# Kernel optimization log

Measured on AMD Instinct MI355X. Metric: run time of the kernel, lower is better.

Reference implementation:

```python
import jax, jax.numpy as jnp
import numpy as np

N_U, N_P, E, E_LAB = 100000, 50000, 2000000, 500000
D_U, D_P, H = 64, 128, 64


def _seg_mean(feat, idx, n):
    # scatter-mean: sum per destination / clamp(count, 1)
    s = jax.ops.segment_sum(feat, idx, num_segments=n)
    c = jax.ops.segment_sum(jnp.ones((idx.shape[0],), feat.dtype), idx, num_segments=n)
    return s / jnp.maximum(c, 1.0)[:, None]


def setup_inputs() -> dict:
    key = jax.random.key(0)
    ks = jax.random.split(key, 16)
    inp = {
        'x_user': jax.random.normal(ks[0], (N_U, D_U), jnp.float32),
        'x_product': jax.random.normal(ks[1], (N_P, D_P), jnp.float32),
        'W1_buys_l': jax.random.normal(ks[2], (D_U, H), jnp.float32) * 0.05,
        'b1_buys': jnp.zeros((H,), jnp.float32),
        'W1_buys_r': jax.random.normal(ks[3], (D_P, H), jnp.float32) * 0.05,
        'W1_rev_l': jax.random.normal(ks[4], (D_P, H), jnp.float32) * 0.05,
        'b1_rev': jnp.zeros((H,), jnp.float32),
        'W1_rev_r': jax.random.normal(ks[5], (D_U, H), jnp.float32) * 0.05,
        'W2_buys_l': jax.random.normal(ks[6], (H, H), jnp.float32) * 0.05,
        'b2_buys': jnp.zeros((H,), jnp.float32),
        'W2_buys_r': jax.random.normal(ks[7], (H, H), jnp.float32) * 0.05,
        'W2_rev_l': jax.random.normal(ks[8], (H, H), jnp.float32) * 0.05,
        'b2_rev': jnp.zeros((H,), jnp.float32),
        'W2_rev_r': jax.random.normal(ks[9], (H, H), jnp.float32) * 0.05,
        'edge_src': jax.random.randint(ks[10], (E,), 0, N_U, jnp.int32),
        'edge_dst': jax.random.randint(ks[11], (E,), 0, N_P, jnp.int32),
        'lab_u': jax.random.randint(ks[12], (E_LAB,), 0, N_U, jnp.int32),
        'lab_p': jax.random.randint(ks[13], (E_LAB,), 0, N_P, jnp.int32),
    }
    return inp


def reference(x_user, x_product, W1_buys_l, b1_buys, W1_buys_r, W1_rev_l, b1_rev, W1_rev_r,
              W2_buys_l, b2_buys, W2_buys_r, W2_rev_l, b2_rev, W2_rev_r,
              edge_src, edge_dst, lab_u, lab_p):
    # SAGEConv (mean aggr): out_dst = mean_agg(x_src) @ W_l + b + x_dst @ W_r
    def sage(x_src, x_dst, src, dst, n_dst, Wl, b, Wr):
        agg = _seg_mean(x_src[src], dst, n_dst)
        return agg @ Wl + b + x_dst @ Wr

    n_u, n_p = x_user.shape[0], x_product.shape[0]
    # layer 1 (per edge type, hetero) + relu
    h_p = jax.nn.relu(sage(x_user, x_product, edge_src, edge_dst, n_p, W1_buys_l, b1_buys, W1_buys_r))
    h_u = jax.nn.relu(sage(x_product, x_user, edge_dst, edge_src, n_u, W1_rev_l, b1_rev, W1_rev_r))
    # layer 2
    h_p2 = sage(h_u, h_p, edge_src, edge_dst, n_p, W2_buys_l, b2_buys, W2_buys_r)
    h_u2 = sage(h_p, h_u, edge_dst, edge_src, n_u, W2_rev_l, b2_rev, W2_rev_r)
    # classifier: per-label-edge dot product
    return jnp.sum(h_u2[lab_u] * h_p2[lab_p], axis=-1)
```

## Files before the change

kernel.cpp:

```cpp
#include <hip/hip_runtime.h>


using u16 = unsigned short;
using u32 = unsigned int;

__device__ __forceinline__ u16 bf16r(float f) {
    u32 b = __float_as_uint(f);
    b += 0x7fffu + ((b >> 16) & 1u);
    return (u16)(b >> 16);
}
__device__ __forceinline__ float bflo(u32 u) { return __uint_as_float(u << 16); }
__device__ __forceinline__ float bfhi(u32 u) { return __uint_as_float(u & 0xffff0000u); }

#define BSH 8
#define MAXB 512
#define CHUNK 4096
#define RPT 16

__global__ __launch_bounds__(256) void k_histA(const int* __restrict__ esrc,
                                               const int* __restrict__ edst,
                                               int* __restrict__ bcntP,
                                               int* __restrict__ bcntU,
                                               int NBP, int NBU, int E) {
    __shared__ int hP[MAXB];
    __shared__ int hU[MAXB];
    int tid = threadIdx.x;
    for (int i = tid; i < MAXB; i += 256) { hP[i] = 0; hU[i] = 0; }
    __syncthreads();
    int E4 = E >> 2;
    const int4* s4 = (const int4*)esrc;
    const int4* d4 = (const int4*)edst;
    int stride = gridDim.x * 256;
    for (int i = blockIdx.x * 256 + tid; i < E4; i += stride) {
        int4 s = s4[i], d = d4[i];
        atomicAdd(&hU[s.x >> BSH], 1); atomicAdd(&hU[s.y >> BSH], 1);
        atomicAdd(&hU[s.z >> BSH], 1); atomicAdd(&hU[s.w >> BSH], 1);
        atomicAdd(&hP[d.x >> BSH], 1); atomicAdd(&hP[d.y >> BSH], 1);
        atomicAdd(&hP[d.z >> BSH], 1); atomicAdd(&hP[d.w >> BSH], 1);
    }
    if (blockIdx.x == 0 && tid < (E & 3)) {
        int e = E4 * 4 + tid;
        atomicAdd(&hU[esrc[e] >> BSH], 1);
        atomicAdd(&hP[edst[e] >> BSH], 1);
    }
    __syncthreads();
    for (int i = tid; i < NBP; i += 256) if (hP[i]) atomicAdd(&bcntP[i], hP[i]);
    for (int i = tid; i < NBU; i += 256) if (hU[i]) atomicAdd(&bcntU[i], hU[i]);
}

__global__ __launch_bounds__(256) void k_scanBuckets(const int* __restrict__ cntP,
                                                     int* __restrict__ basesP,
                                                     int* __restrict__ curP, int NBP,
                                                     const int* __restrict__ cntU,
                                                     int* __restrict__ basesU,
                                                     int* __restrict__ curU, int NBU) {
    const int* cnt; int* bases; int* cur; int NB;
    if (blockIdx.x == 0) { cnt = cntP; bases = basesP; cur = curP; NB = NBP; }
    else                 { cnt = cntU; bases = basesU; cur = curU; NB = NBU; }
    __shared__ int sA[MAXB];
    __shared__ int sB[MAXB];
    int tid = threadIdx.x;
    int v0 = (tid < NB) ? cnt[tid] : 0;
    int v1 = (tid + 256 < NB) ? cnt[tid + 256] : 0;
    sA[tid] = v0; sA[tid + 256] = v1;
    __syncthreads();
    int* src = sA; int* dst = sB;
    for (int off = 1; off < MAXB; off <<= 1) {
        dst[tid] = src[tid] + ((tid >= off) ? src[tid - off] : 0);
        int i2 = tid + 256;
        dst[i2] = src[i2] + ((i2 >= off) ? src[i2 - off] : 0);
        __syncthreads();
        int* t = src; src = dst; dst = t;
    }
    if (tid < NB)       { bases[tid] = src[tid] - v0;             cur[tid] = src[tid] - v0; }
    if (tid + 256 < NB) { bases[tid + 256] = src[tid + 256] - v1; cur[tid + 256] = src[tid + 256] - v1; }
    if (tid == 0) bases[NB] = src[MAXB - 1];
}

__global__ __launch_bounds__(256) void k_partition(const int* __restrict__ keys,
                                                   const int* __restrict__ payload,
                                                   int* __restrict__ cursor,
                                                   uint2* __restrict__ pairs,
                                                   int NB, int E) {
    __shared__ int hist[MAXB];
    __shared__ int sA[MAXB];
    __shared__ int sB[MAXB];
    __shared__ int bx[MAXB];
    __shared__ int gbase[MAXB];
    __shared__ uint2 prs[CHUNK];
    int tid = threadIdx.x;
    int i0 = blockIdx.x * CHUNK;
    int count = min(CHUNK, E - i0);
    for (int i = tid; i < MAXB; i += 256) hist[i] = 0;
    __syncthreads();
    int keyr[RPT], payr[RPT], rankr[RPT];
#pragma unroll
    for (int r = 0; r < RPT; ++r) {
        int idx = r * 256 + tid;
        if (idx < count) {
            int k = keys[i0 + idx];
            keyr[r] = k;
            payr[r] = payload[i0 + idx];
            rankr[r] = atomicAdd(&hist[k >> BSH], 1);
        } else keyr[r] = -1;
    }
    __syncthreads();
    sA[tid] = hist[tid]; sA[tid + 256] = hist[tid + 256];
    __syncthreads();
    int* src = sA; int* dst = sB;
    for (int off = 1; off < MAXB; off <<= 1) {
        dst[tid] = src[tid] + ((tid >= off) ? src[tid - off] : 0);
        int i2 = tid + 256;
        dst[i2] = src[i2] + ((i2 >= off) ? src[i2 - off] : 0);
        __syncthreads();
        int* t = src; src = dst; dst = t;
    }
    bx[tid] = src[tid] - hist[tid];
    bx[tid + 256] = src[tid + 256] - hist[tid + 256];
    __syncthreads();
    for (int b = tid; b < NB; b += 256) {
        int c = hist[b];
        gbase[b] = c ? atomicAdd(&cursor[b], c) : 0;
    }
#pragma unroll
    for (int r = 0; r < RPT; ++r) {
        if (keyr[r] >= 0)
            prs[bx[keyr[r] >> BSH] + rankr[r]] = make_uint2((u32)keyr[r], (u32)payr[r]);
    }
    __syncthreads();
    for (int j = tid; j < count; j += 256) {
        uint2 pr = prs[j];
        int b = pr.x >> BSH;
        pairs[gbase[b] + (j - bx[b])] = pr;
    }
}

__global__ __launch_bounds__(256) void k_bucketFill(
    const uint2* __restrict__ pairsP, const int* __restrict__ basesP, int NBP,
    int* __restrict__ nbr_p, int* __restrict__ deg_p, int* __restrict__ ptr_p, int NP,
    const uint2* __restrict__ pairsU, const int* __restrict__ basesU, int NBU,
    int* __restrict__ nbr_u, int* __restrict__ deg_u, int* __restrict__ ptr_u, int NU) {
    const uint2* pairs; const int* bases; int* nbr; int* deg; int* ptr; int N; int bucket;
    if ((int)blockIdx.x < NBP) {
        pairs = pairsP; bases = basesP; nbr = nbr_p; deg = deg_p; ptr = ptr_p; N = NP;
        bucket = blockIdx.x;
    } else {
        pairs = pairsU; bases = basesU; nbr = nbr_u; deg = deg_u; ptr = ptr_u; N = NU;
        bucket = blockIdx.x - NBP;
    }
    int tid = threadIdx.x;
    int base = bases[bucket];
    int cnt = bases[bucket + 1] - base;
    __shared__ int h[256];
    __shared__ int s[256];
    __shared__ int cur[256];
    h[tid] = 0;
    __syncthreads();
    for (int j = tid; j < cnt; j += 256) atomicAdd(&h[pairs[base + j].x & 255], 1);
    __syncthreads();
    int d = h[tid];
    s[tid] = d;
    __syncthreads();
    for (int off = 1; off < 256; off <<= 1) {
        int v = (tid >= off) ? s[tid - off] : 0;
        __syncthreads();
        s[tid] += v;
        __syncthreads();
    }
    int excl = s[tid] - d;
    int node = bucket * 256 + tid;
    if (node < N) { deg[node] = d; ptr[node] = base + excl; }
    cur[tid] = excl;
    __syncthreads();
    for (int j = tid; j < cnt; j += 256) {
        uint2 pr = pairs[base + j];
        int pos = atomicAdd(&cur[pr.x & 255], 1);
        nbr[base + pos] = pr.y;
    }
}

__global__ __launch_bounds__(256) void k_cast8(const float* __restrict__ x,
                                               u16* __restrict__ y, int n8) {
    int i = blockIdx.x * 256 + threadIdx.x;
    if (i >= n8) return;
    const float4* x4 = (const float4*)x;
    float4 a = x4[i * 2], b = x4[i * 2 + 1];
    uint4 o;
    o.x = (u32)bf16r(a.x) | ((u32)bf16r(a.y) << 16);
    o.y = (u32)bf16r(a.z) | ((u32)bf16r(a.w) << 16);
    o.z = (u32)bf16r(b.x) | ((u32)bf16r(b.y) << 16);
    o.w = (u32)bf16r(b.z) | ((u32)bf16r(b.w) << 16);
    ((uint4*)y)[i] = o;
}

#define ACC8(A0,A1,A2,A3,A4,A5,A6,A7,V) \
    A0 += bflo((V).x); A1 += bfhi((V).x); A2 += bflo((V).y); A3 += bfhi((V).y); \
    A4 += bflo((V).z); A5 += bfhi((V).z); A6 += bflo((V).w); A7 += bfhi((V).w);

__global__ __launch_bounds__(256) void k_gather2(
    const u16* __restrict__ yA, const int* __restrict__ nbrA, const int* __restrict__ stpA,
    const int* __restrict__ degA, float* __restrict__ aggA, int NA,
    const u16* __restrict__ yB, const int* __restrict__ nbrB, const int* __restrict__ stpB,
    const int* __restrict__ degB, float* __restrict__ aggB, int NB) {
    int w = (blockIdx.x * 256 + threadIdx.x) >> 6;
    int lane = threadIdx.x & 63;
    if (w >= NA + NB) return;
    const u16* y; const int* nbr; const int* stp; const int* deg; float* agg; int n;
    if (w < NA) { y = yA; nbr = nbrA; stp = stpA; deg = degA; agg = aggA; n = w; }
    else        { y = yB; nbr = nbrB; stp = stpB; deg = degB; agg = aggB; n = w - NA; }
    const int q = lane >> 3, t = lane & 7;
    const int d = deg[n];
    int j = stp[n];
    const int end = j + d;
    float a0=0,a1=0,a2=0,a3=0,a4=0,a5=0,a6=0,a7=0;
    float b0=0,b1=0,b2=0,b3=0,b4=0,b5=0,b6=0,b7=0;
    float c0=0,c1=0,c2=0,c3=0,c4=0,c5=0,c6=0,c7=0;
    float e0=0,e1=0,e2=0,e3=0,e4=0,e5=0,e6=0,e7=0;
    for (; j + 32 <= end; j += 32) {
        int g0 = nbr[j + q], g1 = nbr[j + 8 + q], g2 = nbr[j + 16 + q], g3 = nbr[j + 24 + q];
        uint4 v0 = *(const uint4*)(y + g0 * 64 + t * 8);
        uint4 v1 = *(const uint4*)(y + g1 * 64 + t * 8);
        uint4 v2 = *(const uint4*)(y + g2 * 64 + t * 8);
        uint4 v3 = *(const uint4*)(y + g3 * 64 + t * 8);
        ACC8(a0,a1,a2,a3,a4,a5,a6,a7,v0);
        ACC8(b0,b1,b2,b3,b4,b5,b6,b7,v1);
        ACC8(c0,c1,c2,c3,c4,c5,c6,c7,v2);
        ACC8(e0,e1,e2,e3,e4,e5,e6,e7,v3);
    }
    for (; j + 16 <= end; j += 16) {
        int g0 = nbr[j + q], g1 = nbr[j + 8 + q];
        uint4 v0 = *(const uint4*)(y + g0 * 64 + t * 8);
        uint4 v1 = *(const uint4*)(y + g1 * 64 + t * 8);
        ACC8(a0,a1,a2,a3,a4,a5,a6,a7,v0);
        ACC8(b0,b1,b2,b3,b4,b5,b6,b7,v1);
    }
    for (; j + 8 <= end; j += 8) {
        int g0 = nbr[j + q];
        uint4 v0 = *(const uint4*)(y + g0 * 64 + t * 8);
        ACC8(a0,a1,a2,a3,a4,a5,a6,a7,v0);
    }
    if (j + q < end) {
        int g0 = nbr[j + q];
        uint4 v0 = *(const uint4*)(y + g0 * 64 + t * 8);
        ACC8(a0,a1,a2,a3,a4,a5,a6,a7,v0);
    }
    a0 += b0 + c0 + e0; a1 += b1 + c1 + e1; a2 += b2 + c2 + e2; a3 += b3 + c3 + e3;
    a4 += b4 + c4 + e4; a5 += b5 + c5 + e5; a6 += b6 + c6 + e6; a7 += b7 + c7 + e7;
#pragma unroll
    for (int m = 8; m < 64; m <<= 1) {
        a0 += __shfl_xor(a0, m, 64); a1 += __shfl_xor(a1, m, 64);
        a2 += __shfl_xor(a2, m, 64); a3 += __shfl_xor(a3, m, 64);
        a4 += __shfl_xor(a4, m, 64); a5 += __shfl_xor(a5, m, 64);
        a6 += __shfl_xor(a6, m, 64); a7 += __shfl_xor(a7, m, 64);
    }
    if (q == 0) {
        float dinv = 1.0f / (float)max(d, 1);
        float* dstp = agg + n * 64 + t * 8;
        *(float4*)dstp       = make_float4(a0 * dinv, a1 * dinv, a2 * dinv, a3 * dinv);
        *(float4*)(dstp + 4) = make_float4(a4 * dinv, a5 * dinv, a6 * dinv, a7 * dinv);
    }
}

#define FMA_ROW(ACC, O, W4) \
    ACC[0] += (O) * (W4).x; ACC[1] += (O) * (W4).y; \
    ACC[2] += (O) * (W4).z; ACC[3] += (O) * (W4).w;

template <int K, int ROWS, bool RELU, bool EMIT, bool PRE, bool BIAS, bool STORE>
__global__ __launch_bounds__(256) void k_ctile(const float* __restrict__ pre,
                                               const float* __restrict__ bias,
                                               const float* __restrict__ x,
                                               const float* __restrict__ W,
                                               float* __restrict__ h,
                                               u16* __restrict__ hbf, int N) {
    constexpr int RR = ROWS / 16;
    constexpr int STRIDE = K + 4;
    constexpr int KF4 = K / 4;
    __shared__ float Ws[K * 64];
    __shared__ float op[ROWS * STRIDE];
    const int tid = threadIdx.x;
    for (int i = tid; i < K * 16; i += 256)
        ((float4*)Ws)[i] = ((const float4*)W)[i];
    const int c4 = (tid & 15) * 4;
    const int rb = (tid >> 4) * RR;
    float bx_ = 0.f, by_ = 0.f, bz_ = 0.f, bw_ = 0.f;
    if (BIAS) {
        float4 b4 = *(const float4*)(bias + c4);
        bx_ = b4.x; by_ = b4.y; bz_ = b4.z; bw_ = b4.w;
    }
    const int ntiles = (N + ROWS - 1) / ROWS;
    for (int tile = blockIdx.x; tile < ntiles; tile += gridDim.x) {
        const int row0 = tile * ROWS;
        __syncthreads();
        for (int i = tid; i < ROWS * KF4; i += 256) {
            int r = i / KF4, k4 = (i % KF4) * 4;
            int row = row0 + r;
            float4 v = make_float4(0.f, 0.f, 0.f, 0.f);
            if (row < N) v = *(const float4*)(x + (size_t)row * K + k4);
            *(float4*)(op + r * STRIDE + k4) = v;
        }
        __syncthreads();
        float acc[RR][4];
#pragma unroll
        for (int i = 0; i < RR; ++i) {
            float px = 0.f, py = 0.f, pz = 0.f, pw = 0.f;
            if (PRE) {
                int row = row0 + rb + i;
                if (row < N) {
                    float4 p = *(const float4*)(pre + row * 64 + c4);
                    px = p.x; py = p.y; pz = p.z; pw = p.w;
                }
            }
            acc[i][0] = bx_ + px; acc[i][1] = by_ + py;
            acc[i][2] = bz_ + pz; acc[i][3] = bw_ + pw;
        }
        for (int kk = 0; kk < K; kk += 4) {
            float4 w0 = *(const float4*)(Ws + (kk + 0) * 64 + c4);
            float4 w1 = *(const float4*)(Ws + (kk + 1) * 64 + c4);
            float4 w2 = *(const float4*)(Ws + (kk + 2) * 64 + c4);
            float4 w3 = *(const float4*)(Ws + (kk + 3) * 64 + c4);
#pragma unroll
            for (int i = 0; i < RR; ++i) {
                float4 o = *(const float4*)(op + (rb + i) * STRIDE + kk);
                FMA_ROW(acc[i], o.x, w0);
                FMA_ROW(acc[i], o.y, w1);
                FMA_ROW(acc[i], o.z, w2);
                FMA_ROW(acc[i], o.w, w3);
            }
        }
#pragma unroll
        for (int i = 0; i < RR; ++i) {
            int row = row0 + rb + i;
            if (row >= N) continue;
            float v0 = acc[i][0], v1 = acc[i][1], v2 = acc[i][2], v3 = acc[i][3];
            if (RELU) {
                v0 = fmaxf(v0, 0.f); v1 = fmaxf(v1, 0.f);
                v2 = fmaxf(v2, 0.f); v3 = fmaxf(v3, 0.f);
            }
            if (STORE)
                *(float4*)(h + row * 64 + c4) = make_float4(v0, v1, v2, v3);
            if (EMIT) {
                uint2 o;
                o.x = (u32)bf16r(v0) | ((u32)bf16r(v1) << 16);
                o.y = (u32)bf16r(v2) | ((u32)bf16r(v3) << 16);
                *(uint2*)(hbf + row * 64 + c4) = o;
            }
        }
    }
}

template <bool PRE, bool BIAS>
__global__ __launch_bounds__(256) void k_ctilePair64(
    const float* __restrict__ pre0, const float* __restrict__ bias0,
    const float* __restrict__ x0, const float* __restrict__ W0,
    float* __restrict__ h0, int N0, int g0,
    const float* __restrict__ pre1, const float* __restrict__ bias1,
    const float* __restrict__ x1, const float* __restrict__ W1,
    float* __restrict__ h1, int N1) {
    constexpr int ROWS = 64, RR = 4, STRIDE = 68, KF4 = 16;
    __shared__ float Ws[64 * 64];
    __shared__ float op[ROWS * STRIDE];
    const float* pre; const float* bias; const float* x; const float* W; float* h;
    int N, bid, gsz;
    if ((int)blockIdx.x < g0) {
        pre = pre0; bias = bias0; x = x0; W = W0; h = h0; N = N0;
        bid = blockIdx.x; gsz = g0;
    } else {
        pre = pre1; bias = bias1; x = x1; W = W1; h = h1; N = N1;
        bid = blockIdx.x - g0; gsz = gridDim.x - g0;
    }
    const int tid = threadIdx.x;
    for (int i = tid; i < 64 * 16; i += 256)
        ((float4*)Ws)[i] = ((const float4*)W)[i];
    const int c4 = (tid & 15) * 4;
    const int rb = (tid >> 4) * RR;
    float bx_ = 0.f, by_ = 0.f, bz_ = 0.f, bw_ = 0.f;
    if (BIAS) {
        float4 b4 = *(const float4*)(bias + c4);
        bx_ = b4.x; by_ = b4.y; bz_ = b4.z; bw_ = b4.w;
    }
    const int ntiles = (N + ROWS - 1) / ROWS;
    for (int tile = bid; tile < ntiles; tile += gsz) {
        const int row0 = tile * ROWS;
        __syncthreads();
        for (int i = tid; i < ROWS * KF4; i += 256) {
            int r = i / KF4, k4 = (i % KF4) * 4;
            int row = row0 + r;
            float4 v = make_float4(0.f, 0.f, 0.f, 0.f);
            if (row < N) v = *(const float4*)(x + (size_t)row * 64 + k4);
            *(float4*)(op + r * STRIDE + k4) = v;
        }
        __syncthreads();
        float acc[RR][4];
#pragma unroll
        for (int i = 0; i < RR; ++i) {
            float px = 0.f, py = 0.f, pz = 0.f, pw = 0.f;
            if (PRE) {
                int row = row0 + rb + i;
                if (row < N) {
                    float4 p = *(const float4*)(pre + row * 64 + c4);
                    px = p.x; py = p.y; pz = p.z; pw = p.w;
                }
            }
            acc[i][0] = bx_ + px; acc[i][1] = by_ + py;
            acc[i][2] = bz_ + pz; acc[i][3] = bw_ + pw;
        }
        for (int kk = 0; kk < 64; kk += 4) {
            float4 w0 = *(const float4*)(Ws + (kk + 0) * 64 + c4);
            float4 w1 = *(const float4*)(Ws + (kk + 1) * 64 + c4);
            float4 w2 = *(const float4*)(Ws + (kk + 2) * 64 + c4);
            float4 w3 = *(const float4*)(Ws + (kk + 3) * 64 + c4);
#pragma unroll
            for (int i = 0; i < RR; ++i) {
                float4 o = *(const float4*)(op + (rb + i) * STRIDE + kk);
                FMA_ROW(acc[i], o.x, w0);
                FMA_ROW(acc[i], o.y, w1);
                FMA_ROW(acc[i], o.z, w2);
                FMA_ROW(acc[i], o.w, w3);
            }
        }
#pragma unroll
        for (int i = 0; i < RR; ++i) {
            int row = row0 + rb + i;
            if (row >= N) continue;
            *(float4*)(h + row * 64 + c4) =
                make_float4(acc[i][0], acc[i][1], acc[i][2], acc[i][3]);
        }
    }
}

__global__ __launch_bounds__(256) void k_classify4(const float* __restrict__ hu,
                                                   const float* __restrict__ hp,
                                                   const int* __restrict__ lu,
                                                   const int* __restrict__ lp,
                                                   float* __restrict__ out, int EL) {
    int w = (blockIdx.x * 256 + threadIdx.x) >> 6;
    int lane = threadIdx.x & 63;
    int q = lane >> 4, t = lane & 15;
    int e = w * 4 + q;
    float v = 0.f;
    if (e < EL) {
        int u = lu[e], p = lp[e];
        float4 a = *(const float4*)(hu + u * 64 + t * 4);
        float4 b = *(const float4*)(hp + p * 64 + t * 4);
        v = a.x * b.x + a.y * b.y + a.z * b.z + a.w * b.w;
    }
#pragma unroll
    for (int m = 1; m < 16; m <<= 1) v += __shfl_xor(v, m, 64);
    if (t == 0 && e < EL) out[e] = v;
}

extern "C" void kernel_launch(void* const* d_in, const int* in_sizes, int n_in,
                              void* d_out, int out_size, void* d_ws, size_t ws_size,
                              hipStream_t stream) {
    const float* x_user    = (const float*)d_in[0];
    const float* x_product = (const float*)d_in[1];
    const float* W1bl = (const float*)d_in[2];
    const float* b1b  = (const float*)d_in[3];
    const float* W1br = (const float*)d_in[4];
    const float* W1rl = (const float*)d_in[5];
    const float* b1r  = (const float*)d_in[6];
    const float* W1rr = (const float*)d_in[7];
    const float* W2bl = (const float*)d_in[8];
    const float* b2b  = (const float*)d_in[9];
    const float* W2br = (const float*)d_in[10];
    const float* W2rl = (const float*)d_in[11];
    const float* b2r  = (const float*)d_in[12];
    const float* W2rr = (const float*)d_in[13];
    const int* esrc = (const int*)d_in[14];
    const int* edst = (const int*)d_in[15];
    const int* lu   = (const int*)d_in[16];
    const int* lp   = (const int*)d_in[17];

    const int NU = in_sizes[0] / 64;
    const int NP = in_sizes[1] / 128;
    const int E  = in_sizes[14];
    const int EL = in_sizes[16];
    const int NBP = (NP + 255) >> BSH;
    const int NBU = (NU + 255) >> BSH;

    char* ws = (char*)d_ws;
    size_t off = 0;
    auto alloc = [&](size_t bytes) -> void* {
        void* p = ws + off;
        off += (bytes + 255) & ~(size_t)255;
        return p;
    };
    int*   deg_u  = (int*)alloc((size_t)NU * 4);
    int*   deg_p  = (int*)alloc((size_t)NP * 4);
    int*   ptr_u  = (int*)alloc((size_t)NU * 4);
    int*   ptr_p  = (int*)alloc((size_t)NP * 4);
    int*   bcntP  = (int*)alloc((size_t)MAXB * 4);
    int*   bcntU  = (int*)alloc((size_t)MAXB * 4);
    int*   basesP = (int*)alloc((size_t)(MAXB + 1) * 4);
    int*   basesU = (int*)alloc((size_t)(MAXB + 1) * 4);
    int*   curP   = (int*)alloc((size_t)MAXB * 4);
    int*   curU   = (int*)alloc((size_t)MAXB * 4);
    int*   nbr_u  = (int*)alloc((size_t)E * 4);
    int*   nbr_p  = (int*)alloc((size_t)E * 4);
    size_t aggBytes = (size_t)(NP + NU) * 64 * 4;
    size_t pairBytes = (size_t)E * 8 * 2;
    char* uni = (char*)alloc(aggBytes > pairBytes ? aggBytes : pairBytes);
    float* aggP   = (float*)uni;
    float* aggU   = (float*)(uni + (size_t)NP * 64 * 4);
    uint2* pairsP = (uint2*)uni;
    uint2* pairsU = (uint2*)(uni + (size_t)E * 8);
    u16*   bfA    = (u16*)alloc((size_t)NU * 64 * 2);
    u16*   bfB    = (u16*)alloc((size_t)NP * 64 * 2);
    float* h_p    = (float*)alloc((size_t)NP * 64 * 4);
    float* h_u    = (float*)alloc((size_t)NU * 64 * 4);

    hipMemsetAsync(bcntP, 0, (size_t)MAXB * 2 * 4, stream);
    k_histA<<<512, 256, 0, stream>>>(esrc, edst, bcntP, bcntU, NBP, NBU, E);
    k_scanBuckets<<<2, 256, 0, stream>>>(bcntP, basesP, curP, NBP, bcntU, basesU, curU, NBU);
    const int pblocks = (E + CHUNK - 1) / CHUNK;
    k_partition<<<pblocks, 256, 0, stream>>>(edst, esrc, curP, pairsP, NBP, E);
    k_partition<<<pblocks, 256, 0, stream>>>(esrc, edst, curU, pairsU, NBU, E);
    k_bucketFill<<<NBP + NBU, 256, 0, stream>>>(pairsP, basesP, NBP, nbr_p, deg_p, ptr_p, NP,
                                                pairsU, basesU, NBU, nbr_u, deg_u, ptr_u, NU);

    k_cast8<<<(NU * 64 / 8 + 255) / 256, 256, 0, stream>>>(x_user, bfA, NU * 64 / 8);
    {
        const int tiles = (NP + 31) / 32;
        k_ctile<128, 32, false, true, false, false, false><<<(tiles < 768 ? tiles : 768), 256, 0, stream>>>(
            nullptr, nullptr, x_product, W1rl, nullptr, bfB, NP);
    }

    const int tP64 = (NP + 63) / 64, tP32 = (NP + 31) / 32;
    const int tU64 = (NU + 63) / 64;
    auto cap = [](int t, int c) { return t < c ? t : c; };
    const int gP = cap(tP64, 512), gU = cap(tU64, 512);

    k_gather2<<<(NP + NU + 3) / 4, 256, 0, stream>>>(bfA, nbr_p, ptr_p, deg_p, aggP, NP,
                                                     bfB, nbr_u, ptr_u, deg_u, aggU, NU);
    k_ctile<64, 64, false, false, false, true, true><<<cap(tP64, 1024), 256, 0, stream>>>(
        nullptr, b1b, aggP, W1bl, h_p, nullptr, NP);
    k_ctile<128, 32, true, true, true, false, true><<<cap(tP32, 768), 256, 0, stream>>>(
        h_p, nullptr, x_product, W1br, h_p, bfB, NP);
    k_ctile<64, 64, true, true, true, true, true><<<cap(tU64, 1024), 256, 0, stream>>>(
        aggU, b1r, x_user, W1rr, h_u, bfA, NU);

    k_gather2<<<(NP + NU + 3) / 4, 256, 0, stream>>>(bfA, nbr_p, ptr_p, deg_p, aggP, NP,
                                                     bfB, nbr_u, ptr_u, deg_u, aggU, NU);
    k_ctilePair64<false, true><<<gP + gU, 256, 0, stream>>>(
        nullptr, b2b, aggP, W2bl, aggP, NP, gP,
        nullptr, b2r, aggU, W2rl, aggU, NU);
    k_ctilePair64<true, false><<<gP + gU, 256, 0, stream>>>(
        aggP, nullptr, h_p, W2br, h_p, NP, gP,
        aggU, nullptr, h_u, W2rr, h_u, NU);

    k_classify4<<<((EL + 3) / 4 + 3) / 4, 256, 0, stream>>>(h_u, h_p, lu, lp, (float*)d_out, EL);
}
```

Measured before the change: 548.7 us.

## Store aggregates and final embeddings in bf16 to cut memory traffic

```diff
diff --git a/kernel.cpp b/kernel.cpp
--- a/kernel.cpp
+++ b/kernel.cpp
@@ -199,13 +199,13 @@
 
 __global__ __launch_bounds__(256) void k_gather2(
     const u16* __restrict__ yA, const int* __restrict__ nbrA, const int* __restrict__ stpA,
-    const int* __restrict__ degA, float* __restrict__ aggA, int NA,
+    const int* __restrict__ degA, u16* __restrict__ aggA, int NA,
     const u16* __restrict__ yB, const int* __restrict__ nbrB, const int* __restrict__ stpB,
-    const int* __restrict__ degB, float* __restrict__ aggB, int NB) {
+    const int* __restrict__ degB, u16* __restrict__ aggB, int NB) {
     int w = (blockIdx.x * 256 + threadIdx.x) >> 6;
     int lane = threadIdx.x & 63;
     if (w >= NA + NB) return;
-    const u16* y; const int* nbr; const int* stp; const int* deg; float* agg; int n;
+    const u16* y; const int* nbr; const int* stp; const int* deg; u16* agg; int n;
     if (w < NA) { y = yA; nbr = nbrA; stp = stpA; deg = degA; agg = aggA; n = w; }
     else        { y = yB; nbr = nbrB; stp = stpB; deg = degB; agg = aggB; n = w - NA; }
     const int q = lane >> 3, t = lane & 7;
@@ -255,9 +255,12 @@
     }
     if (q == 0) {
         float dinv = 1.0f / (float)max(d, 1);
-        float* dstp = agg + n * 64 + t * 8;
-        *(float4*)dstp       = make_float4(a0 * dinv, a1 * dinv, a2 * dinv, a3 * dinv);
-        *(float4*)(dstp + 4) = make_float4(a4 * dinv, a5 * dinv, a6 * dinv, a7 * dinv);
+        uint4 o;
+        o.x = (u32)bf16r(a0 * dinv) | ((u32)bf16r(a1 * dinv) << 16);
+        o.y = (u32)bf16r(a2 * dinv) | ((u32)bf16r(a3 * dinv) << 16);
+        o.z = (u32)bf16r(a4 * dinv) | ((u32)bf16r(a5 * dinv) << 16);
+        o.w = (u32)bf16r(a6 * dinv) | ((u32)bf16r(a7 * dinv) << 16);
+        *(uint4*)(agg + n * 64 + t * 8) = o;
     }
 }
 
@@ -265,10 +268,11 @@
     ACC[0] += (O) * (W4).x; ACC[1] += (O) * (W4).y; \
     ACC[2] += (O) * (W4).z; ACC[3] += (O) * (W4).w;
 
-template <int K, int ROWS, bool RELU, bool EMIT, bool PRE, bool BIAS, bool STORE>
-__global__ __launch_bounds__(256) void k_ctile(const float* __restrict__ pre,
+template <int K, int ROWS, bool RELU, bool EMIT, bool PRE, bool BIAS, bool STORE,
+          bool XBF16, bool PREBF16>
+__global__ __launch_bounds__(256) void k_ctile(const void* __restrict__ prev,
                                                const float* __restrict__ bias,
-                                               const float* __restrict__ x,
+                                               const void* __restrict__ xv,
                                                const float* __restrict__ W,
                                                float* __restrict__ h,
                                                u16* __restrict__ hbf, int N) {
@@ -295,7 +299,14 @@
             int r = i / KF4, k4 = (i % KF4) * 4;
             int row = row0 + r;
             float4 v = make_float4(0.f, 0.f, 0.f, 0.f);
-            if (row < N) v = *(const float4*)(x + (size_t)row * K + k4);
+            if (row < N) {
+                if (XBF16) {
+                    uint2 u = *(const uint2*)((const u16*)xv + (size_t)row * K + k4);
+                    v = make_float4(bflo(u.x), bfhi(u.x), bflo(u.y), bfhi(u.y));
+                } else {
+                    v = *(const float4*)((const float*)xv + (size_t)row * K + k4);
+                }
+            }
             *(float4*)(op + r * STRIDE + k4) = v;
         }
         __syncthreads();
@@ -306,8 +317,13 @@
             if (PRE) {
                 int row = row0 + rb + i;
                 if (row < N) {
-                    float4 p = *(const float4*)(pre + row * 64 + c4);
-                    px = p.x; py = p.y; pz = p.z; pw = p.w;
+                    if (PREBF16) {
+                        uint2 u = *(const uint2*)((const u16*)prev + (size_t)row * 64 + c4);
+                        px = bflo(u.x); py = bfhi(u.x); pz = bflo(u.y); pw = bfhi(u.y);
+                    } else {
+                        float4 p = *(const float4*)((const float*)prev + (size_t)row * 64 + c4);
+                        px = p.x; py = p.y; pz = p.z; pw = p.w;
+                    }
                 }
             }
             acc[i][0] = bx_ + px; acc[i][1] = by_ + py;
@@ -348,24 +364,25 @@
     }
 }
 
-template <bool PRE, bool BIAS>
+template <bool XBF16, bool PRE, bool BIAS, bool EMIT, bool STORE>
 __global__ __launch_bounds__(256) void k_ctilePair64(
     const float* __restrict__ pre0, const float* __restrict__ bias0,
-    const float* __restrict__ x0, const float* __restrict__ W0,
-    float* __restrict__ h0, int N0, int g0,
+    const void* __restrict__ x0, const float* __restrict__ W0,
+    float* __restrict__ h0, u16* __restrict__ hbf0, int N0, int g0,
     const float* __restrict__ pre1, const float* __restrict__ bias1,
-    const float* __restrict__ x1, const float* __restrict__ W1,
-    float* __restrict__ h1, int N1) {
+    const void* __restrict__ x1, const float* __restrict__ W1,
+    float* __restrict__ h1, u16* __restrict__ hbf1, int N1) {
     constexpr int ROWS = 64, RR = 4, STRIDE = 68, KF4 = 16;
     __shared__ float Ws[64 * 64];
     __shared__ float op[ROWS * STRIDE];
-    const float* pre; const float* bias; const float* x; const float* W; float* h;
+    const float* pre; const float* bias; const void* x; const float* W;
+    float* h; u16* hbf;
     int N, bid, gsz;
     if ((int)blockIdx.x < g0) {
-        pre = pre0; bias = bias0; x = x0; W = W0; h = h0; N = N0;
+        pre = pre0; bias = bias0; x = x0; W = W0; h = h0; hbf = hbf0; N = N0;
         bid = blockIdx.x; gsz = g0;
     } else {
-        pre = pre1; bias = bias1; x = x1; W = W1; h = h1; N = N1;
+        pre = pre1; bias = bias1; x = x1; W = W1; h = h1; hbf = hbf1; N = N1;
         bid = blockIdx.x - g0; gsz = gridDim.x - g0;
     }
     const int tid = threadIdx.x;
@@ -386,7 +403,14 @@
             int r = i / KF4, k4 = (i % KF4) * 4;
             int row = row0 + r;
             float4 v = make_float4(0.f, 0.f, 0.f, 0.f);
-            if (row < N) v = *(const float4*)(x + (size_t)row * 64 + k4);
+            if (row < N) {
+                if (XBF16) {
+                    uint2 u = *(const uint2*)((const u16*)x + (size_t)row * 64 + k4);
+                    v = make_float4(bflo(u.x), bfhi(u.x), bflo(u.y), bfhi(u.y));
+                } else {
+                    v = *(const float4*)((const float*)x + (size_t)row * 64 + k4);
+                }
+            }
             *(float4*)(op + r * STRIDE + k4) = v;
         }
         __syncthreads();
@@ -397,7 +421,7 @@
             if (PRE) {
                 int row = row0 + rb + i;
                 if (row < N) {
-                    float4 p = *(const float4*)(pre + row * 64 + c4);
+                    float4 p = *(const float4*)(pre + (size_t)row * 64 + c4);
                     px = p.x; py = p.y; pz = p.z; pw = p.w;
                 }
             }
@@ -422,17 +446,24 @@
         for (int i = 0; i < RR; ++i) {
             int row = row0 + rb + i;
             if (row >= N) continue;
-            *(float4*)(h + row * 64 + c4) =
-                make_float4(acc[i][0], acc[i][1], acc[i][2], acc[i][3]);
-        }
-    }
-}
-
-__global__ __launch_bounds__(256) void k_classify4(const float* __restrict__ hu,
-                                                   const float* __restrict__ hp,
-                                                   const int* __restrict__ lu,
-                                                   const int* __restrict__ lp,
-                                                   float* __restrict__ out, int EL) {
+            float v0 = acc[i][0], v1 = acc[i][1], v2 = acc[i][2], v3 = acc[i][3];
+            if (STORE)
+                *(float4*)(h + row * 64 + c4) = make_float4(v0, v1, v2, v3);
+            if (EMIT) {
+                uint2 o;
+                o.x = (u32)bf16r(v0) | ((u32)bf16r(v1) << 16);
+                o.y = (u32)bf16r(v2) | ((u32)bf16r(v3) << 16);
+                *(uint2*)(hbf + row * 64 + c4) = o;
+            }
+        }
+    }
+}
+
+__global__ __launch_bounds__(256) void k_classify4b(const u16* __restrict__ hu,
+                                                    const u16* __restrict__ hp,
+                                                    const int* __restrict__ lu,
+                                                    const int* __restrict__ lp,
+                                                    float* __restrict__ out, int EL) {
     int w = (blockIdx.x * 256 + threadIdx.x) >> 6;
     int lane = threadIdx.x & 63;
     int q = lane >> 4, t = lane & 15;
@@ -440,9 +471,10 @@
     float v = 0.f;
     if (e < EL) {
         int u = lu[e], p = lp[e];
-        float4 a = *(const float4*)(hu + u * 64 + t * 4);
-        float4 b = *(const float4*)(hp + p * 64 + t * 4);
-        v = a.x * b.x + a.y * b.y + a.z * b.z + a.w * b.w;
+        uint2 a = *(const uint2*)(hu + u * 64 + t * 4);
+        uint2 b = *(const uint2*)(hp + p * 64 + t * 4);
+        v = bflo(a.x) * bflo(b.x) + bfhi(a.x) * bfhi(b.x)
+          + bflo(a.y) * bflo(b.y) + bfhi(a.y) * bfhi(b.y);
     }
 #pragma unroll
     for (int m = 1; m < 16; m <<= 1) v += __shfl_xor(v, m, 64);
@@ -497,11 +529,14 @@
     int*   curU   = (int*)alloc((size_t)MAXB * 4);
     int*   nbr_u  = (int*)alloc((size_t)E * 4);
     int*   nbr_p  = (int*)alloc((size_t)E * 4);
-    size_t aggBytes = (size_t)(NP + NU) * 64 * 4;
-    size_t pairBytes = (size_t)E * 8 * 2;
-    char* uni = (char*)alloc(aggBytes > pairBytes ? aggBytes : pairBytes);
-    float* aggP   = (float*)uni;
-    float* aggU   = (float*)(uni + (size_t)NP * 64 * 4);
+    size_t needA = (size_t)(NP + NU) * 64 * 2
+                 + (size_t)(NP + NU) * 64 * 4;
+    size_t needB = (size_t)E * 8 * 2;
+    char* uni = (char*)alloc(needA > needB ? needA : needB);
+    u16*   aggP   = (u16*)uni;
+    u16*   aggU   = (u16*)(uni + (size_t)NP * 64 * 2);
+    float* tmpP   = (float*)(uni + (size_t)(NP + NU) * 64 * 2);
+    float* tmpU   = (float*)(uni + (size_t)(NP + NU) * 64 * 2 + (size_t)NP * 64 * 4);
     uint2* pairsP = (uint2*)uni;
     uint2* pairsU = (uint2*)(uni + (size_t)E * 8);
     u16*   bfA    = (u16*)alloc((size_t)NU * 64 * 2);
@@ -521,7 +556,8 @@
     k_cast8<<<(NU * 64 / 8 + 255) / 256, 256, 0, stream>>>(x_user, bfA, NU * 64 / 8);
     {
         const int tiles = (NP + 31) / 32;
-        k_ctile<128, 32, false, true, false, false, false><<<(tiles < 768 ? tiles : 768), 256, 0, stream>>>(
+        k_ctile<128, 32, false, true, false, false, false, false, false>
+            <<<(tiles < 768 ? tiles : 768), 256, 0, stream>>>(
             nullptr, nullptr, x_product, W1rl, nullptr, bfB, NP);
     }
 
@@ -532,21 +568,24 @@
 
     k_gather2<<<(NP + NU + 3) / 4, 256, 0, stream>>>(bfA, nbr_p, ptr_p, deg_p, aggP, NP,
                                                      bfB, nbr_u, ptr_u, deg_u, aggU, NU);
-    k_ctile<64, 64, false, false, false, true, true><<<cap(tP64, 1024), 256, 0, stream>>>(
+    k_ctile<64, 64, false, false, false, true, true, true, false>
+        <<<cap(tP64, 1024), 256, 0, stream>>>(
         nullptr, b1b, aggP, W1bl, h_p, nullptr, NP);
-    k_ctile<128, 32, true, true, true, false, true><<<cap(tP32, 768), 256, 0, stream>>>(
+    k_ctile<128, 32, true, true, true, false, true, false, false>
+        <<<cap(tP32, 768), 256, 0, stream>>>(
         h_p, nullptr, x_product, W1br, h_p, bfB, NP);
-    k_ctile<64, 64, true, true, true, true, true><<<cap(tU64, 1024), 256, 0, stream>>>(
+    k_ctile<64, 64, true, true, true, true, true, false, true>
+        <<<cap(tU64, 1024), 256, 0, stream>>>(
         aggU, b1r, x_user, W1rr, h_u, bfA, NU);
 
     k_gather2<<<(NP + NU + 3) / 4, 256, 0, stream>>>(bfA, nbr_p, ptr_p, deg_p, aggP, NP,
                                                      bfB, nbr_u, ptr_u, deg_u, aggU, NU);
-    k_ctilePair64<false, true><<<gP + gU, 256, 0, stream>>>(
-        nullptr, b2b, aggP, W2bl, aggP, NP, gP,
-        nullptr, b2r, aggU, W2rl, aggU, NU);
-    k_ctilePair64<true, false><<<gP + gU, 256, 0, stream>>>(
-        aggP, nullptr, h_p, W2br, h_p, NP, gP,
-        aggU, nullptr, h_u, W2rr, h_u, NU);
-
-    k_classify4<<<((EL + 3) / 4 + 3) / 4, 256, 0, stream>>>(h_u, h_p, lu, lp, (float*)d_out, EL);
-}
+    k_ctilePair64<true, false, true, false, true><<<gP + gU, 256, 0, stream>>>(
+        nullptr, b2b, aggP, W2bl, tmpP, nullptr, NP, gP,
+        nullptr, b2r, aggU, W2rl, tmpU, nullptr, NU);
+    k_ctilePair64<false, true, false, true, false><<<gP + gU, 256, 0, stream>>>(
+        tmpP, nullptr, h_p, W2br, nullptr, bfB, NP, gP,
+        tmpU, nullptr, h_u, W2rr, nullptr, bfA, NU);
+
+    k_classify4b<<<((EL + 3) / 4 + 3) / 4, 256, 0, stream>>>(bfA, bfB, lu, lp, (float*)d_out, EL);
+}
```

Measured after the change: 590.5 us. 7.6% more time.
